# Optimization experiments

Measured on AMD Instinct MI355X. Metric: run time of the kernel, lower is better.

Reference implementation:

```python
import jax, jax.numpy as jnp
import numpy as np

B, N, D = 4, 1024, 1024
H, HD = 16, 64  # num_heads, head_dim


def rotate_half(x):
    x1, x2 = jnp.split(x, 2, axis=-1)
    return jnp.concatenate([-x2, x1], axis=-1)


def setup_inputs() -> dict:
    key = jax.random.key(0)
    ks = jax.random.split(key, 10)
    s = 1.0 / np.sqrt(D)
    hidden_states = jax.random.normal(ks[0], (B, N, D), jnp.float32)
    # rotary angles -> cos/sin per position per head-dim
    ang = jax.random.uniform(ks[1], (B, N, HD), jnp.float32, 0.0, 2 * np.pi)
    cos, sin = jnp.cos(ang), jnp.sin(ang)
    wq = jax.random.normal(ks[2], (D, D), jnp.float32) * s
    bq = jnp.zeros((D,), jnp.float32)
    wk = jax.random.normal(ks[3], (D, D), jnp.float32) * s  # key_bias=False
    wv = jax.random.normal(ks[4], (D, D), jnp.float32) * s
    bv = jnp.zeros((D,), jnp.float32)
    wo = jax.random.normal(ks[5], (D, D), jnp.float32) * s
    bo = jnp.zeros((D,), jnp.float32)
    return {"hidden_states": hidden_states, "cos": cos, "sin": sin,
            "wq": wq, "bq": bq, "wk": wk, "wv": wv, "bv": bv,
            "wo": wo, "bo": bo}


def reference(hidden_states, cos, sin, wq, bq, wk, wv, bv, wo, bo):
    # weights are (out, in) as in eqx Linear: y = x @ W.T + b
    q = jnp.einsum('bnd,ed->bne', hidden_states, wq) + bq
    k = jnp.einsum('bnd,ed->bne', hidden_states, wk)
    v = jnp.einsum('bnd,ed->bne', hidden_states, wv) + bv
    # [B, H, N, HD]
    q = q.reshape(B, N, H, HD).transpose(0, 2, 1, 3)
    k = k.reshape(B, N, H, HD).transpose(0, 2, 1, 3)
    v = v.reshape(B, N, H, HD).transpose(0, 2, 1, 3)
    c = cos[:, None, :, :]  # broadcast over heads
    s = sin[:, None, :, :]
    q = q * c + rotate_half(q) * s
    k = k * c + rotate_half(k) * s
    scale = 1.0 / np.sqrt(HD)
    scores = jnp.einsum('bhqd,bhkd->bhqk', q, k) * scale
    attn = jax.nn.softmax(scores, axis=-1)
    out = jnp.einsum('bhqk,bhkd->bhqd', attn, v)
    out = out.transpose(0, 2, 1, 3).reshape(B, N, D)
    return jnp.einsum('bnd,ed->bne', out, wo) + bo
```

## Files before the change

kernel.cpp:

```cpp
#include <hip/hip_runtime.h>
#include <hip/hip_bf16.h>
#include <cstdint>


typedef _Float16 half8 __attribute__((ext_vector_type(8)));
typedef _Float16 half4 __attribute__((ext_vector_type(4)));
typedef float f32x4 __attribute__((ext_vector_type(4)));

#define DEV_INLINE __device__ __forceinline__

constexpr int Bb = 4, Ns = 1024, Dd = 1024, Hh = 16, HDd = 64;
constexpr int M_ROWS = Bb * Ns;
constexpr int EQKV = 3 * Dd;

constexpr size_t OFF_HSH  = 0;
constexpr size_t SZ_HSH   = (size_t)M_ROWS * Dd * 2;
constexpr size_t OFF_WQKV = OFF_HSH + SZ_HSH;
constexpr size_t SZ_WQKV  = (size_t)EQKV * Dd * 2;
constexpr size_t OFF_WO   = OFF_WQKV + SZ_WQKV;
constexpr size_t SZ_WO    = (size_t)Dd * Dd * 2;
constexpr size_t OFF_BIAS = OFF_WO + SZ_WO;
constexpr size_t OFF_ATTN = OFF_BIAS + 16384;
constexpr size_t SZ_HEADS = (size_t)Bb * Hh * Ns * HDd * 2;
constexpr size_t OFF_QT   = OFF_ATTN + SZ_HEADS;
constexpr size_t OFF_KT   = OFF_QT + SZ_HEADS;
constexpr size_t OFF_VT   = OFF_KT + SZ_HEADS;

DEV_INLINE void async_cp16(const _Float16* g, _Float16* l) {
  __builtin_amdgcn_global_load_lds(
      (const __attribute__((address_space(1))) unsigned int*)(g),
      (__attribute__((address_space(3))) unsigned int*)(l), 16, 0, 0);
}

DEV_INLINE half4 cvt4(float4 v) {
  half4 h;
  h[0] = (_Float16)v.x; h[1] = (_Float16)v.y;
  h[2] = (_Float16)v.z; h[3] = (_Float16)v.w;
  return h;
}

__global__ __launch_bounds__(256) void cvt_kernel(
    const float* __restrict__ hs, const float* __restrict__ wq,
    const float* __restrict__ wk, const float* __restrict__ wv,
    const float* __restrict__ wo, const float* __restrict__ bq,
    const float* __restrict__ bv, _Float16* __restrict__ hsH,
    _Float16* __restrict__ wqkvH, _Float16* __restrict__ woH,
    float* __restrict__ biasP)
{
  const int gid = blockIdx.x * 256 + threadIdx.x;
  const int nHs4 = M_ROWS * Dd / 4;
  const int nW4  = 3 * Dd * Dd / 4;
  const int nWo4 = Dd * Dd / 4;
  if (gid < EQKV / 4) {
#pragma unroll
    for (int j = 0; j < 4; ++j) {
      int e = gid * 4 + j;
      biasP[e] = (e < 1024) ? bq[e] : (e < 2048 ? 0.f : bv[e - 2048]);
    }
  }
  if (gid < nHs4) {
    float4 v = reinterpret_cast<const float4*>(hs)[gid];
    reinterpret_cast<half4*>(hsH)[gid] = cvt4(v);
  } else if (gid < nHs4 + nW4) {
    int j = gid - nHs4;
    const int per = Dd * Dd / 4;
    const float* src = (j < per) ? wq : (j < 2 * per ? wk : wv);
    float4 v = reinterpret_cast<const float4*>(src)[j % per];
    reinterpret_cast<half4*>(wqkvH)[j] = cvt4(v);
  } else if (gid < nHs4 + nW4 + nWo4) {
    int j = gid - nHs4 - nW4;
    float4 v = reinterpret_cast<const float4*>(wo)[j];
    reinterpret_cast<half4*>(woH)[j] = cvt4(v);
  }
}

template<int MODE, int BN>
__global__ __launch_bounds__(256, 3) void gemm_bt(
    const _Float16* __restrict__ A, const _Float16* __restrict__ Bt,
    const float* __restrict__ bias, void* __restrict__ out,
    const float* __restrict__ cosp, const float* __restrict__ sinp,
    _Float16* __restrict__ qT, _Float16* __restrict__ kT,
    int M, int E, int K)
{
  constexpr int JW = BN / 32;
  __shared__ _Float16 As[128 * 64];
  __shared__ _Float16 Bs[BN * 64];
  const int t = threadIdx.x;
  const int lane = t & 63, wave = t >> 6;
  const int c15 = lane & 15, g = lane >> 4;
  const int wm = wave >> 1, wn = wave & 1;
  const int m0 = blockIdx.y * 128, e0 = blockIdx.x * BN;

  const int srow  = t >> 3;
  const int scol8 = ((t & 7) ^ ((t >> 3) & 7)) * 8;
  const _Float16* gA0 = A  + (size_t)(m0 + srow) * K + scol8;
  const _Float16* gB0 = Bt + (size_t)(e0 + srow) * K + scol8;
  char* lA = (char*)As + wave * 1024;
  char* lB = (char*)Bs + wave * 1024;

  const char* pA[4][2];
  const char* pB[JW][2];
#pragma unroll
  for (int mi = 0; mi < 4; ++mi)
#pragma unroll
    for (int kh = 0; kh < 2; ++kh) {
      int ra = wm * 64 + mi * 16 + c15;
      pA[mi][kh] = (const char*)As + ra * 128 + (((kh * 4 + g) ^ (ra & 7)) << 4);
    }
#pragma unroll
  for (int j = 0; j < JW; ++j)
#pragma unroll
    for (int kh = 0; kh < 2; ++kh) {
      int rb = wn * (BN / 2) + j * 16 + c15;
      pB[j][kh] = (const char*)Bs + rb * 128 + (((kh * 4 + g) ^ (rb & 7)) << 4);
    }

  f32x4 acc[4][JW];
  const f32x4 zero = {0.f, 0.f, 0.f, 0.f};
#pragma unroll
  for (int i = 0; i < 4; ++i)
#pragma unroll
    for (int j = 0; j < JW; ++j) acc[i][j] = zero;

  const int nk = K >> 6;
  for (int kt = 0; kt < nk; ++kt) {
    const _Float16* ga = gA0 + kt * 64;
    const _Float16* gb = gB0 + kt * 64;
#pragma unroll
    for (int i = 0; i < 4; ++i)
      async_cp16(ga + (size_t)(32 * i) * K, (_Float16*)(lA + i * 4096));
#pragma unroll
    for (int i = 0; i < BN / 32; ++i)
      async_cp16(gb + (size_t)(32 * i) * K, (_Float16*)(lB + i * 4096));
    __syncthreads();
#pragma unroll
    for (int kh = 0; kh < 2; ++kh) {
      half8 a[4], b[JW];
#pragma unroll
      for (int i = 0; i < 4; ++i) a[i] = *reinterpret_cast<const half8*>(pA[i][kh]);
#pragma unroll
      for (int j = 0; j < JW; ++j) b[j] = *reinterpret_cast<const half8*>(pB[j][kh]);
#pragma unroll
      for (int i = 0; i < 4; ++i)
#pragma unroll
        for (int j = 0; j < JW; ++j)
          acc[i][j] = __builtin_amdgcn_mfma_f32_16x16x32_f16(a[i], b[j], acc[i][j], 0, 0, 0);
    }
    __syncthreads();
  }

  if (MODE == 1) {
#pragma unroll
    for (int i = 0; i < 4; ++i)
#pragma unroll
      for (int j = 0; j < JW; ++j)
#pragma unroll
        for (int r = 0; r < 4; ++r) {
          int row = m0 + wm * 64 + i * 16 + g * 4 + r;
          int col = e0 + wn * (BN / 2) + j * 16 + c15;
          reinterpret_cast<float*>(out)[(size_t)row * E + col] =
              acc[i][j][r] + bias[col];
        }
  } else {
    const int scol = e0 + wn * 64;
    const int sec = scol >> 10;
    const int h = (scol & 1023) >> 6;
    const int bh = (m0 >> 10) * Hh + h;
    if (sec < 2) {
      _Float16* dst = sec ? kT : qT;
#pragma unroll
      for (int i = 0; i < 4; ++i)
#pragma unroll
        for (int r = 0; r < 4; ++r) {
          int row = m0 + wm * 64 + i * 16 + g * 4 + r;
          size_t obase = ((size_t)bh * Ns + (row & 1023)) * HDd;
          const float* cb = cosp + (size_t)row * HDd;
          const float* sb = sinp + (size_t)row * HDd;
#pragma unroll
          for (int j = 0; j < 2; ++j) {
            int hd = j * 16 + c15;
            float x1 = acc[i][j][r]     + bias[scol + hd];
            float x2 = acc[i][j + 2][r] + bias[scol + hd + 32];
            float c1 = cb[hd],      s1 = sb[hd];
            float c2 = cb[hd + 32], s2 = sb[hd + 32];
            dst[obase + hd]      = (_Float16)(x1 * c1 - x2 * s1);
            dst[obase + hd + 32] = (_Float16)(x2 * c2 + x1 * s2);
          }
        }
    } else {
      _Float16* vTo = (_Float16*)out;
      _Float16* vbase = vTo + (size_t)bh * (HDd * Ns) + (m0 & 1023) + wm * 64;
#pragma unroll
      for (int i = 0; i < 4; ++i)
#pragma unroll
        for (int j = 0; j < 4; ++j) {
          int hd = j * 16 + c15;
          float bv_ = bias[scol + hd];
          half4 pk;
#pragma unroll
          for (int r = 0; r < 4; ++r) pk[r] = (_Float16)(acc[i][j][r] + bv_);
          *reinterpret_cast<half4*>(vbase + (size_t)hd * Ns + i * 16 + g * 4) = pk;
        }
    }
  }
}

__global__ __launch_bounds__(256, 2) void attn_kernel(
    const _Float16* __restrict__ qT, const _Float16* __restrict__ kT,
    const _Float16* __restrict__ vT, _Float16* __restrict__ attnH)
{
  __shared__ _Float16 Ks[2][64 * 64];
  __shared__ _Float16 Vst[2][64 * 64];
  __shared__ _Float16 Ps[128 * 64];
  const int t = threadIdx.x;
  const int lane = t & 63, wave = t >> 6;
  const int c = lane & 15, g = lane >> 4;
  const int bx = blockIdx.x;
  const int qt = bx & 7, bh = bx >> 3;
  const int b = bh >> 4, h = bh & 15;
  const int qn0 = qt * 128;
  const int wq0 = wave * 32;

  half8 qf[2][2];
#pragma unroll
  for (int s16 = 0; s16 < 2; ++s16) {
    const _Float16* qp =
        qT + ((size_t)bh * Ns + qn0 + wq0 + s16 * 16 + c) * HDd + g * 8;
    qf[s16][0] = *reinterpret_cast<const half8*>(qp);
    qf[s16][1] = *reinterpret_cast<const half8*>(qp + 32);
  }

  half8 ones;
#pragma unroll
  for (int j = 0; j < 8; ++j) ones[j] = (_Float16)1.0f;

  f32x4 accO[2][4];
  f32x4 accL[2];
  const f32x4 zero = {0.f, 0.f, 0.f, 0.f};
#pragma unroll
  for (int s16 = 0; s16 < 2; ++s16) {
    accL[s16] = zero;
#pragma unroll
    for (int d = 0; d < 4; ++d) accO[s16][d] = zero;
  }

  const int srow = t >> 3, sch = t & 7;
  const int ssw = (sch * 16) ^ ((srow & 7) << 4);
  const _Float16* gK = kT + ((size_t)bh * Ns + srow) * HDd + sch * 8;
  const _Float16* gV = vT + ((size_t)bh * HDd + srow) * Ns + sch * 8;
  char* wKa = (char*)Ks[0]  + srow * 128 + ssw;
  char* wVa = (char*)Vst[0] + srow * 128 + ssw;

  const char* pK[2][4];
  const char* pV[2][4];
  const char* pP[2][2];
#pragma unroll
  for (int ks = 0; ks < 2; ++ks) {
#pragma unroll
    for (int i = 0; i < 4; ++i) {
      int rowk = i * 16 + c;
      pK[ks][i] = (const char*)Ks[0]  + rowk * 128 + ((ks * 64 + g * 16) ^ ((rowk & 7) << 4));
      pV[ks][i] = (const char*)Vst[0] + rowk * 128 + ((ks * 64 + g * 16) ^ ((rowk & 7) << 4));
    }
#pragma unroll
    for (int s16 = 0; s16 < 2; ++s16) {
      int rowp = wq0 + s16 * 16 + c;
      pP[s16][ks] = (const char*)Ps + rowp * 128 + ((ks * 64 + g * 16) ^ ((rowp & 7) << 4));
    }
  }

  const float K1 = 0.18033688011112042f;
  const float K2 = -11.541560327111707f;
  char* prow0 = (char*)Ps + (wq0 + c) * 128;
  const int psw = (c & 7) << 4;

  {
    half8 k0 = *reinterpret_cast<const half8*>(gK);
    half8 k1 = *reinterpret_cast<const half8*>(gK + 32 * HDd);
    half8 v0 = *reinterpret_cast<const half8*>(gV);
    half8 v1 = *reinterpret_cast<const half8*>(gV + 32 * Ns);
    *reinterpret_cast<half8*>(wKa) = k0;
    *reinterpret_cast<half8*>(wKa + 4096) = k1;
    *reinterpret_cast<half8*>(wVa) = v0;
    *reinterpret_cast<half8*>(wVa + 4096) = v1;
  }
  __syncthreads();

  for (int jt = 0; jt < 16; ++jt) {
    const int bo = (jt & 1) * 8192;
    const bool pre = (jt + 1 < 16);
    half8 kr0, kr1, vr0, vr1;
    if (pre) {
      kr0 = *reinterpret_cast<const half8*>(gK + (jt + 1) * 4096);
      kr1 = *reinterpret_cast<const half8*>(gK + (jt + 1) * 4096 + 32 * HDd);
      vr0 = *reinterpret_cast<const half8*>(gV + (jt + 1) * 64);
      vr1 = *reinterpret_cast<const half8*>(gV + (jt + 1) * 64 + 32 * Ns);
    }

    f32x4 s[2][4];
#pragma unroll
    for (int s16 = 0; s16 < 2; ++s16)
#pragma unroll
      for (int i = 0; i < 4; ++i) s[s16][i] = zero;
    __builtin_amdgcn_s_setprio(1);
#pragma unroll
    for (int ks = 0; ks < 2; ++ks) {
      half8 kf[4];
#pragma unroll
      for (int i = 0; i < 4; ++i)
        kf[i] = *reinterpret_cast<const half8*>(pK[ks][i] + bo);
#pragma unroll
      for (int i = 0; i < 4; ++i) {
        s[0][i] = __builtin_amdgcn_mfma_f32_16x16x32_f16(kf[i], qf[0][ks], s[0][i], 0, 0, 0);
        s[1][i] = __builtin_amdgcn_mfma_f32_16x16x32_f16(kf[i], qf[1][ks], s[1][i], 0, 0, 0);
      }
    }
    __builtin_amdgcn_s_setprio(0);

#pragma unroll
    for (int s16 = 0; s16 < 2; ++s16) {
      char* prow = prow0 + s16 * 2048;
#pragma unroll
      for (int i = 0; i < 4; ++i) {
        half4 pk;
        pk[0] = (_Float16)__builtin_amdgcn_exp2f(fmaf(s[s16][i][0], K1, K2));
        pk[1] = (_Float16)__builtin_amdgcn_exp2f(fmaf(s[s16][i][1], K1, K2));
        pk[2] = (_Float16)__builtin_amdgcn_exp2f(fmaf(s[s16][i][2], K1, K2));
        pk[3] = (_Float16)__builtin_amdgcn_exp2f(fmaf(s[s16][i][3], K1, K2));
        *reinterpret_cast<half4*>(prow + ((i * 32 + g * 8) ^ psw)) = pk;
      }
    }

    __builtin_amdgcn_s_setprio(1);
#pragma unroll
    for (int ks = 0; ks < 2; ++ks) {
      half8 pa0 = *reinterpret_cast<const half8*>(pP[0][ks]);
      half8 pa1 = *reinterpret_cast<const half8*>(pP[1][ks]);
      accL[0] = __builtin_amdgcn_mfma_f32_16x16x32_f16(pa0, ones, accL[0], 0, 0, 0);
      accL[1] = __builtin_amdgcn_mfma_f32_16x16x32_f16(pa1, ones, accL[1], 0, 0, 0);
#pragma unroll
      for (int dt = 0; dt < 4; ++dt) {
        half8 vf = *reinterpret_cast<const half8*>(pV[ks][dt] + bo);
        accO[0][dt] = __builtin_amdgcn_mfma_f32_16x16x32_f16(pa0, vf, accO[0][dt], 0, 0, 0);
        accO[1][dt] = __builtin_amdgcn_mfma_f32_16x16x32_f16(pa1, vf, accO[1][dt], 0, 0, 0);
      }
    }
    __builtin_amdgcn_s_setprio(0);

    if (pre) {
      const int wo_ = 8192 - bo;
      *reinterpret_cast<half8*>(wKa + wo_) = kr0;
      *reinterpret_cast<half8*>(wKa + wo_ + 4096) = kr1;
      *reinterpret_cast<half8*>(wVa + wo_) = vr0;
      *reinterpret_cast<half8*>(wVa + wo_ + 4096) = vr1;
      __syncthreads();
    }
  }

#pragma unroll
  for (int s16 = 0; s16 < 2; ++s16)
#pragma unroll
    for (int r = 0; r < 4; ++r) {
      float inv = 1.f / accL[s16][r];
      int n = qn0 + wq0 + s16 * 16 + g * 4 + r;
#pragma unroll
      for (int dt = 0; dt < 4; ++dt) {
        float v = accO[s16][dt][r] * inv;
        attnH[((size_t)b * Ns + n) * Dd + h * HDd + dt * 16 + c] = (_Float16)v;
      }
    }
}

extern "C" void kernel_launch(void* const* d_in, const int* in_sizes, int n_in,
                              void* d_out, int out_size, void* d_ws, size_t ws_size,
                              hipStream_t stream) {
  const float* hs   = (const float*)d_in[0];
  const float* cosp = (const float*)d_in[1];
  const float* sinp = (const float*)d_in[2];
  const float* wq   = (const float*)d_in[3];
  const float* bq   = (const float*)d_in[4];
  const float* wk   = (const float*)d_in[5];
  const float* wv   = (const float*)d_in[6];
  const float* bv   = (const float*)d_in[7];
  const float* wo   = (const float*)d_in[8];
  const float* bo   = (const float*)d_in[9];

  char* ws = (char*)d_ws;
  _Float16* hsH   = (_Float16*)(ws + OFF_HSH);
  _Float16* wqkvH = (_Float16*)(ws + OFF_WQKV);
  _Float16* woH   = (_Float16*)(ws + OFF_WO);
  float*    biasP = (float*)(ws + OFF_BIAS);
  _Float16* attnH = (_Float16*)(ws + OFF_ATTN);
  _Float16* qTp   = (_Float16*)(ws + OFF_QT);
  _Float16* kTp   = (_Float16*)(ws + OFF_KT);
  _Float16* vTp   = (_Float16*)(ws + OFF_VT);

  cvt_kernel<<<8192, 256, 0, stream>>>(hs, wq, wk, wv, wo, bq, bv,
                                       hsH, wqkvH, woH, biasP);
  gemm_bt<0, 128><<<dim3(EQKV / 128, M_ROWS / 128), 256, 0, stream>>>(
      hsH, wqkvH, biasP, vTp, cosp, sinp, qTp, kTp, M_ROWS, EQKV, Dd);
  attn_kernel<<<Bb * Hh * (Ns / 128), 256, 0, stream>>>(qTp, kTp, vTp, attnH);
  gemm_bt<1, 64><<<dim3(Dd / 64, M_ROWS / 128), 256, 0, stream>>>(
      attnH, woH, bo, d_out, nullptr, nullptr, nullptr, nullptr,
      M_ROWS, Dd, Dd);
}
```

Measured before the change: 95.25 us.

## Rewrite QKV GEMM as 256x256 tile, 8-wave kernel with 4-stage async pipeline

Replaces the templated QKV projection GEMM with a dedicated kernel using 512 threads, 256x256 output tiles, and a 4-buffer LDS ring filled three K-steps ahead via async copies with explicit vmcnt waits. It also raises wave priority around the MFMA block. The aim is to improve data reuse per tile and hide global load latency behind compute. The catch is a grid of only 12x16=192 blocks, which may underfill the device, plus heavy register pressure from 32 accumulators per thread. The output GEMM is split into its own non-templated kernel with the same logic.

```diff
diff --git a/kernel.cpp b/kernel.cpp
--- a/kernel.cpp
+++ b/kernel.cpp
@@ -74,15 +74,123 @@
   }
 }
 
-template<int MODE, int BN>
-__global__ __launch_bounds__(256, 3) void gemm_bt(
+__global__ __launch_bounds__(512, 2) void gemm_qkv8(
     const _Float16* __restrict__ A, const _Float16* __restrict__ Bt,
-    const float* __restrict__ bias, void* __restrict__ out,
+    const float* __restrict__ bias, _Float16* __restrict__ vTo,
     const float* __restrict__ cosp, const float* __restrict__ sinp,
-    _Float16* __restrict__ qT, _Float16* __restrict__ kT,
+    _Float16* __restrict__ qT, _Float16* __restrict__ kT)
+{
+  __shared__ _Float16 AsP[4 * 256 * 32];
+  __shared__ _Float16 BsP[4 * 256 * 32];
+  constexpr int Kc = 1024;
+  const int t = threadIdx.x;
+  const int lane = t & 63, wave = t >> 6;
+  const int c = lane & 15, g = lane >> 4;
+  const int wm = wave >> 2, wn = wave & 3;
+  const int m0 = blockIdx.y * 256, e0 = blockIdx.x * 256;
+
+  const int scol8 = ((t & 3) ^ ((t >> 3) & 3)) * 8;
+  const _Float16* gA0 = A  + (size_t)(m0 + (t >> 2)) * Kc + scol8;
+  const _Float16* gB0 = Bt + (size_t)(e0 + (t >> 2)) * Kc + scol8;
+  char* ldsA = (char*)AsP;
+  char* ldsB = (char*)BsP;
+  const int wb = wave * 1024;
+
+  auto stage = [&](int tt) {
+    char* la = ldsA + (tt & 3) * 16384 + wb;
+    char* lb = ldsB + (tt & 3) * 16384 + wb;
+    const _Float16* ga = gA0 + tt * 32;
+    const _Float16* gb = gB0 + tt * 32;
+    async_cp16(ga, (_Float16*)la);
+    async_cp16(ga + (size_t)128 * Kc, (_Float16*)(la + 8192));
+    async_cp16(gb, (_Float16*)lb);
+    async_cp16(gb + (size_t)128 * Kc, (_Float16*)(lb + 8192));
+  };
+
+  const int swz16 = (g ^ ((c >> 1) & 3)) << 4;
+  const int offA0 = (wm * 128 + c) * 64 + swz16;
+  const int offB0 = (wn * 64 + c) * 64 + swz16;
+
+  f32x4 acc[8][4];
+  const f32x4 zero = {0.f, 0.f, 0.f, 0.f};
+#pragma unroll
+  for (int mi = 0; mi < 8; ++mi)
+#pragma unroll
+    for (int j = 0; j < 4; ++j) acc[mi][j] = zero;
+
+  stage(0); stage(1); stage(2);
+
+  for (int tt = 0; tt < 32; ++tt) {
+    __builtin_amdgcn_s_barrier();
+    if (tt < 30)       asm volatile("s_waitcnt vmcnt(8)" ::: "memory");
+    else if (tt == 30) asm volatile("s_waitcnt vmcnt(4)" ::: "memory");
+    else               asm volatile("s_waitcnt vmcnt(0)" ::: "memory");
+    if (tt < 29) stage(tt + 3);
+
+    const char* bA = ldsA + (tt & 3) * 16384;
+    const char* bB = ldsB + (tt & 3) * 16384;
+    half8 bf[4];
+#pragma unroll
+    for (int j = 0; j < 4; ++j)
+      bf[j] = *reinterpret_cast<const half8*>(bB + offB0 + j * 1024);
+    __builtin_amdgcn_s_setprio(1);
+#pragma unroll
+    for (int mi = 0; mi < 8; ++mi) {
+      half8 a = *reinterpret_cast<const half8*>(bA + offA0 + mi * 1024);
+#pragma unroll
+      for (int j = 0; j < 4; ++j)
+        acc[mi][j] = __builtin_amdgcn_mfma_f32_16x16x32_f16(a, bf[j], acc[mi][j], 0, 0, 0);
+    }
+    __builtin_amdgcn_s_setprio(0);
+  }
+
+  const int scol = e0 + wn * 64;
+  const int sec = scol >> 10;
+  const int h = (scol & 1023) >> 6;
+  const int bh = (m0 >> 10) * Hh + h;
+  if (sec < 2) {
+    _Float16* dst = sec ? kT : qT;
+#pragma unroll
+    for (int mi = 0; mi < 8; ++mi)
+#pragma unroll
+      for (int r = 0; r < 4; ++r) {
+        int row = m0 + wm * 128 + mi * 16 + g * 4 + r;
+        size_t obase = ((size_t)bh * Ns + (row & 1023)) * HDd;
+        const float* cb = cosp + (size_t)row * HDd;
+        const float* sb = sinp + (size_t)row * HDd;
+#pragma unroll
+        for (int j = 0; j < 2; ++j) {
+          int hd = j * 16 + c;
+          float x1 = acc[mi][j][r]     + bias[scol + hd];
+          float x2 = acc[mi][j + 2][r] + bias[scol + hd + 32];
+          float c1 = cb[hd],      s1 = sb[hd];
+          float c2 = cb[hd + 32], s2 = sb[hd + 32];
+          dst[obase + hd]      = (_Float16)(x1 * c1 - x2 * s1);
+          dst[obase + hd + 32] = (_Float16)(x2 * c2 + x1 * s2);
+        }
+      }
+  } else {
+    _Float16* vbase = vTo + (size_t)bh * (HDd * Ns) + (m0 & 1023) + wm * 128;
+#pragma unroll
+    for (int mi = 0; mi < 8; ++mi)
+#pragma unroll
+      for (int j = 0; j < 4; ++j) {
+        int hd = j * 16 + c;
+        float bv_ = bias[scol + hd];
+        half4 pk;
+#pragma unroll
+        for (int r = 0; r < 4; ++r) pk[r] = (_Float16)(acc[mi][j][r] + bv_);
+        *reinterpret_cast<half4*>(vbase + (size_t)hd * Ns + mi * 16 + g * 4) = pk;
+      }
+  }
+}
+
+__global__ __launch_bounds__(256, 3) void gemm_out(
+    const _Float16* __restrict__ A, const _Float16* __restrict__ Bt,
+    const float* __restrict__ bias, float* __restrict__ out,
     int M, int E, int K)
 {
-  constexpr int JW = BN / 32;
+  constexpr int BN = 64, JW = 2;
   __shared__ _Float16 As[128 * 64];
   __shared__ _Float16 Bs[BN * 64];
   const int t = threadIdx.x;
@@ -149,60 +257,16 @@
     __syncthreads();
   }
 
-  if (MODE == 1) {
-#pragma unroll
-    for (int i = 0; i < 4; ++i)
-#pragma unroll
-      for (int j = 0; j < JW; ++j)
-#pragma unroll
-        for (int r = 0; r < 4; ++r) {
-          int row = m0 + wm * 64 + i * 16 + g * 4 + r;
-          int col = e0 + wn * (BN / 2) + j * 16 + c15;
-          reinterpret_cast<float*>(out)[(size_t)row * E + col] =
-              acc[i][j][r] + bias[col];
-        }
-  } else {
-    const int scol = e0 + wn * 64;
-    const int sec = scol >> 10;
-    const int h = (scol & 1023) >> 6;
-    const int bh = (m0 >> 10) * Hh + h;
-    if (sec < 2) {
-      _Float16* dst = sec ? kT : qT;
-#pragma unroll
-      for (int i = 0; i < 4; ++i)
-#pragma unroll
-        for (int r = 0; r < 4; ++r) {
-          int row = m0 + wm * 64 + i * 16 + g * 4 + r;
-          size_t obase = ((size_t)bh * Ns + (row & 1023)) * HDd;
-          const float* cb = cosp + (size_t)row * HDd;
-          const float* sb = sinp + (size_t)row * HDd;
-#pragma unroll
-          for (int j = 0; j < 2; ++j) {
-            int hd = j * 16 + c15;
-            float x1 = acc[i][j][r]     + bias[scol + hd];
-            float x2 = acc[i][j + 2][r] + bias[scol + hd + 32];
-            float c1 = cb[hd],      s1 = sb[hd];
-            float c2 = cb[hd + 32], s2 = sb[hd + 32];
-            dst[obase + hd]      = (_Float16)(x1 * c1 - x2 * s1);
-            dst[obase + hd + 32] = (_Float16)(x2 * c2 + x1 * s2);
-          }
-        }
-    } else {
-      _Float16* vTo = (_Float16*)out;
-      _Float16* vbase = vTo + (size_t)bh * (HDd * Ns) + (m0 & 1023) + wm * 64;
-#pragma unroll
-      for (int i = 0; i < 4; ++i)
-#pragma unroll
-        for (int j = 0; j < 4; ++j) {
-          int hd = j * 16 + c15;
-          float bv_ = bias[scol + hd];
-          half4 pk;
-#pragma unroll
-          for (int r = 0; r < 4; ++r) pk[r] = (_Float16)(acc[i][j][r] + bv_);
-          *reinterpret_cast<half4*>(vbase + (size_t)hd * Ns + i * 16 + g * 4) = pk;
-        }
-    }
-  }
+#pragma unroll
+  for (int i = 0; i < 4; ++i)
+#pragma unroll
+    for (int j = 0; j < JW; ++j)
+#pragma unroll
+      for (int r = 0; r < 4; ++r) {
+        int row = m0 + wm * 64 + i * 16 + g * 4 + r;
+        int col = e0 + wn * (BN / 2) + j * 16 + c15;
+        out[(size_t)row * E + col] = acc[i][j][r] + bias[col];
+      }
 }
 
 __global__ __launch_bounds__(256, 2) void attn_kernel(
@@ -397,10 +461,9 @@
 
   cvt_kernel<<<8192, 256, 0, stream>>>(hs, wq, wk, wv, wo, bq, bv,
                                        hsH, wqkvH, woH, biasP);
-  gemm_bt<0, 128><<<dim3(EQKV / 128, M_ROWS / 128), 256, 0, stream>>>(
-      hsH, wqkvH, biasP, vTp, cosp, sinp, qTp, kTp, M_ROWS, EQKV, Dd);
+  gemm_qkv8<<<dim3(EQKV / 256, M_ROWS / 256), 512, 0, stream>>>(
+      hsH, wqkvH, biasP, vTp, cosp, sinp, qTp, kTp);
   attn_kernel<<<Bb * Hh * (Ns / 128), 256, 0, stream>>>(qTp, kTp, vTp, attnH);
-  gemm_bt<1, 64><<<dim3(Dd / 64, M_ROWS / 128), 256, 0, stream>>>(
-      attnH, woH, bo, d_out, nullptr, nullptr, nullptr, nullptr,
-      M_ROWS, Dd, Dd);
-}
+  gemm_out<<<dim3(Dd / 64, M_ROWS / 128), 256, 0, stream>>>(
+      attnH, woH, bo, (float*)d_out, M_ROWS, Dd, Dd);
+}
```

After: 110.5 us. 1.16x slower.
